# Kernel optimization log

Measured on AMD Instinct MI355X. Metric: run time of the kernel, lower is better.

The kernel has to match this reference:

```python
import jax, jax.numpy as jnp
import numpy as np

B, F, H, L, K = 16384, 1024, 1024, 256, 7

def _lin(key, fi, fo, lead=()):
    k1, k2 = jax.random.split(key)
    s = 1.0 / np.sqrt(fi)
    W = jax.random.uniform(k1, lead + (fi, fo), jnp.float32, -s, s)
    b = jax.random.uniform(k2, lead + (fo,), jnp.float32, -s, s)
    return W, b

def setup_inputs() -> dict:
    ks = jax.random.split(jax.random.key(0), 16)
    x = jax.random.normal(ks[0], (B, F), jnp.float32)
    t = jax.random.randint(ks[1], (B,), 0, K, jnp.int32)
    y = jax.random.normal(ks[2], (B,), jnp.float32)
    d = jax.random.normal(ks[3], (B,), jnp.float32)
    tw0, tb0 = _lin(ks[4], F, L)
    tw1, tb1 = _lin(ks[5], L, L)
    tw2, tb2 = _lin(ks[6], L, K)
    yw0, yb0 = _lin(ks[7], F, H)
    yw1, yb1 = _lin(ks[8], H, H)
    yhW, yhb = _lin(ks[9], H, 2, (K,))
    dw0, db0 = _lin(ks[10], F, H)
    dw1, db1 = _lin(ks[11], H, H)
    dhW, dhb = _lin(ks[12], H, 2, (K,))
    zw0, zb0 = _lin(ks[13], F + 2, H)
    zw1, zb1 = _lin(ks[14], H, H)
    zhW, zhb = _lin(ks[15], H, 2 * L, (K,))
    return dict(x=x, t=t, y=y, d=d, tw0=tw0, tb0=tb0, tw1=tw1, tb1=tb1, tw2=tw2, tb2=tb2,
                yw0=yw0, yb0=yb0, yw1=yw1, yb1=yb1, yhW=yhW, yhb=yhb,
                dw0=dw0, db0=db0, dw1=dw1, db1=db1, dhW=dhW, dhb=dhb,
                zw0=zw0, zb0=zb0, zw1=zw1, zb1=zb1, zhW=zhW, zhb=zhb)

def _mlp2(x, w0, b0, w1, b1):
    # FullyConnected([in, H, H], final_activation=ELU)
    return jax.nn.elu(jax.nn.elu(x @ w0 + b0) @ w1 + b1)

def _select(hidden, t, hW, hb):
    # dense compute of all K treatment heads, then per-row gather by t
    all_out = jnp.einsum('bh,khd->bkd', hidden, hW) + hb  # [B, K, D]
    return jnp.take_along_axis(all_out, t[:, None, None], axis=1)[:, 0]

def _normal_head(sel):
    # pyro NormalNet head on a scalar outcome
    loc = jnp.clip(sel[:, 0:1], -1e6, 1e6)
    scale = jnp.minimum(jax.nn.softplus(sel[:, 1:2]) + 1e-3, 1e6)
    return loc, scale

def _diagnormal_head(sel):
    loc = jnp.clip(sel[:, :L], -100.0, 100.0)
    scale = jnp.minimum(jax.nn.softplus(sel[:, L:]) + 0.001, 100.0)
    return loc, scale

def reference(x, t, y, d, tw0, tb0, tw1, tb1, tw2, tb2,
              yw0, yb0, yw1, yb1, yhW, yhb,
              dw0, db0, dw1, db1, dhW, dhb,
              zw0, zb0, zw1, zb1, zhW, zhb):
    # t_nn: MultinormNet, ELU final activation then clamp(-10, 10)
    t_logits = jnp.clip(jax.nn.elu(_mlp2(x, tw0, tb0, tw1, tb1) @ tw2 + tb2), -10.0, 10.0)
    # y_dist(t, x)
    hy = _mlp2(x, yw0, yb0, yw1, yb1)
    y_loc, y_scale = _normal_head(_select(hy, t, yhW, yhb))
    # d_dist(t, x)
    hd = _mlp2(x, dw0, db0, dw1, db1)
    d_loc, d_scale = _normal_head(_select(hd, t, dhW, dhb))
    # z_dist(y, d, t, x): hidden from cat([y, d, x])
    hz = _mlp2(jnp.concatenate([y[:, None], d[:, None], x], axis=-1), zw0, zb0, zw1, zb1)
    z_loc, z_scale = _diagnormal_head(_select(hz, t, zhW, zhb))
    # [B, K + 4 + 2L]
    return jnp.concatenate([t_logits, y_loc, y_scale, d_loc, d_scale, z_loc, z_scale], axis=-1)
```

## Files before the change

kernel.cpp:

```cpp
#include <hip/hip_runtime.h>
#include <hip/hip_bf16.h>
#include <cstdint>
#include <cstddef>

typedef __hip_bfloat16 bf16;
typedef __bf16 bf16x8 __attribute__((ext_vector_type(8)));
typedef float f32x4 __attribute__((ext_vector_type(4)));

#define DEVFN static __device__ __forceinline__
#define SBAR() __builtin_amdgcn_s_barrier()
#define VMCNT(n) asm volatile("s_waitcnt vmcnt(" #n ")" ::: "memory")

DEVFN void async16(const void* g, void* l) {
  __builtin_amdgcn_global_load_lds(
      (const __attribute__((address_space(1))) uint32_t*)g,
      (__attribute__((address_space(3))) uint32_t*)l, 16, 0, 0);
}

DEVFN float eluf(float v) { return v > 0.f ? v : expm1f(v); }
DEVFN float softplusf(float x) {
  return x > 0.f ? x + log1pf(expf(-x)) : log1pf(expf(x));
}


DEVFN void stage_half(const bf16* p, int ld, bf16* reg, int tid) {
  async16(p, reg + tid * 8);
  async16(p + (size_t)64 * ld, reg + 4096 + tid * 8);
}

template <int PART>
DEVFN void stage_ht(const bf16* pA, const bf16* pB, int lda, int ldb,
                    bf16* lds, int tid, int t) {
  bf16* base = lds + (t & 1) * 32768;
  if constexpr (PART == 0)
    stage_half(pA + (size_t)t * 64, lda, base, tid);
  else if constexpr (PART == 1)
    stage_half(pA + (size_t)t * 64 + (size_t)128 * lda, lda, base + 8192, tid);
  else if constexpr (PART == 2)
    stage_half(pB + (size_t)t * 64, ldb, base + 16384, tid);
  else
    stage_half(pB + (size_t)t * 64 + (size_t)128 * ldb, ldb, base + 24576, tid);
}

template <int MB, int NB>
DEVFN void mfma4(f32x4 (&acc)[8][4], const bf16x8 (&af)[4][2],
                 const bf16x8 (&bv)[2][2]) {
#pragma unroll
  for (int mf = 0; mf < 4; ++mf)
#pragma unroll
    for (int nf = 0; nf < 2; ++nf) {
      acc[MB + mf][NB + nf] = __builtin_amdgcn_mfma_f32_16x16x32_bf16(
          af[mf][0], bv[nf][0], acc[MB + mf][NB + nf], 0, 0, 0);
      acc[MB + mf][NB + nf] = __builtin_amdgcn_mfma_f32_16x16x32_bf16(
          af[mf][1], bv[nf][1], acc[MB + mf][NB + nf], 0, 0, 0);
    }
}

DEVFN void quad_phases(const bf16* Ab, const bf16* Bb, int cs0, int cs1,
                       f32x4 (&acc)[8][4], const bf16* pA, const bf16* pB,
                       int lda, int ldb, bf16* lds, int tid,
                       int t, bool st1, bool st2, int vmend) {
  bf16x8 af[4][2], b0[2][2], b1[2][2];
#pragma unroll
  for (int mf = 0; mf < 4; ++mf) {
    af[mf][0] = *(const bf16x8*)(Ab + mf * 1024 + cs0);
    af[mf][1] = *(const bf16x8*)(Ab + mf * 1024 + cs1);
  }
#pragma unroll
  for (int nf = 0; nf < 2; ++nf) {
    b0[nf][0] = *(const bf16x8*)(Bb + nf * 1024 + cs0);
    b0[nf][1] = *(const bf16x8*)(Bb + nf * 1024 + cs1);
  }
  if (st1) stage_ht<3>(pA, pB, lda, ldb, lds, tid, t + 1);
  SBAR();
  __builtin_amdgcn_s_setprio(1);
  mfma4<0, 0>(acc, af, b0);
  __builtin_amdgcn_s_setprio(0);
  SBAR();
#pragma unroll
  for (int nf = 0; nf < 2; ++nf) {
    b1[nf][0] = *(const bf16x8*)(Bb + (2 + nf) * 1024 + cs0);
    b1[nf][1] = *(const bf16x8*)(Bb + (2 + nf) * 1024 + cs1);
  }
  if (st1) stage_ht<1>(pA, pB, lda, ldb, lds, tid, t + 1);
  SBAR();
  __builtin_amdgcn_s_setprio(1);
  mfma4<0, 2>(acc, af, b1);
  __builtin_amdgcn_s_setprio(0);
  SBAR();
#pragma unroll
  for (int mf = 0; mf < 4; ++mf) {
    af[mf][0] = *(const bf16x8*)(Ab + (4 + mf) * 1024 + cs0);
    af[mf][1] = *(const bf16x8*)(Ab + (4 + mf) * 1024 + cs1);
  }
  if (st2) stage_ht<2>(pA, pB, lda, ldb, lds, tid, t + 2);
  SBAR();
  __builtin_amdgcn_s_setprio(1);
  mfma4<4, 0>(acc, af, b0);
  __builtin_amdgcn_s_setprio(0);
  SBAR();
  if (st2) stage_ht<0>(pA, pB, lda, ldb, lds, tid, t + 2);
  SBAR();
  __builtin_amdgcn_s_setprio(1);
  mfma4<4, 2>(acc, af, b1);
  __builtin_amdgcn_s_setprio(0);
  if (vmend == 0) { VMCNT(0); }
  else if (vmend > 0) { VMCNT(4); }
  SBAR();
}

DEVFN void gemm256(const bf16* pA, const bf16* pB, int lda, int ldb, int NT,
                   bf16* lds, int tid, int wm, int wn, int quad, int l15,
                   f32x4 (&acc)[8][4]) {
  const int k7 = l15 & 7;
  const int cs0 = (quad ^ k7) * 8;
  const int cs1 = cs0 ^ 32;
  const bf16* Abase = lds + wm * 8192 + l15 * 64;
  const bf16* Bbase = lds + 16384 + (wn >> 1) * 8192 + ((wn & 1) * 64 + l15) * 64;
  stage_ht<0>(pA, pB, lda, ldb, lds, tid, 0);
  stage_ht<1>(pA, pB, lda, ldb, lds, tid, 0);
  stage_ht<2>(pA, pB, lda, ldb, lds, tid, 0);
  stage_ht<3>(pA, pB, lda, ldb, lds, tid, 0);
  stage_ht<2>(pA, pB, lda, ldb, lds, tid, 1);
  stage_ht<0>(pA, pB, lda, ldb, lds, tid, 1);
  VMCNT(4);
  SBAR();
  const int NI = NT >> 1;
  for (int j = 0; j < NI; ++j) {
    const bool last = (j == NI - 1);
    const int a = 2 * j;
    quad_phases(Abase, Bbase, cs0, cs1, acc, pA, pB, lda, ldb, lds, tid,
                a, true, !last, last ? 0 : 4);
    quad_phases(Abase + 32768, Bbase + 32768, cs0, cs1, acc, pA, pB, lda, ldb,
                lds, tid, a + 1, !last, !last, last ? -1 : 4);
  }
}

template <int NAH, int NBH, int NFB>
DEVFN void kloop32(const bf16* (&gA)[NAH], const bf16* (&gB)[NBH], bf16* As,
                   bf16* Bs, int tid, const bf16* aBase, const bf16* bBase,
                   int colsel, f32x4 (&acc)[4][NFB], int kiters) {
  for (int kt = 0; kt < kiters; ++kt) {
#pragma unroll
    for (int c = 0; c < NAH; ++c) async16(gA[c], As + c * 2048 + tid * 8);
#pragma unroll
    for (int c = 0; c < NBH; ++c) async16(gB[c], Bs + c * 2048 + tid * 8);
#pragma unroll
    for (int c = 0; c < NAH; ++c) gA[c] += 32;
#pragma unroll
    for (int c = 0; c < NBH; ++c) gB[c] += 32;
    __syncthreads();
    bf16x8 af[4], bfv[NFB];
#pragma unroll
    for (int r = 0; r < 4; ++r) af[r] = *(const bf16x8*)(aBase + r * 512 + colsel);
#pragma unroll
    for (int c = 0; c < NFB; ++c) bfv[c] = *(const bf16x8*)(bBase + c * 512 + colsel);
#pragma unroll
    for (int r = 0; r < 4; ++r)
#pragma unroll
      for (int c = 0; c < NFB; ++c)
        acc[r][c] = __builtin_amdgcn_mfma_f32_16x16x32_bf16(af[r], bfv[c], acc[r][c], 0, 0, 0);
    __syncthreads();
  }
}

DEVFN int swz_scol(int tid) { return (((tid & 3) ^ ((tid >> 3) & 3)) * 8); }
DEVFN int swz_colsel(int quad, int l15) { return ((quad ^ ((l15 >> 1) & 3)) * 8); }

DEVFN void transpose_tile(const float* src, bf16* dst, int R, int C, int bx, int by) {
  __shared__ float tile[32][33];
  const int c0 = bx * 32, r0 = by * 32;
  const int tx = threadIdx.x & 31, ty = threadIdx.x >> 5;
#pragma unroll
  for (int rr = ty; rr < 32; rr += 8)
    tile[rr][tx] = src[(size_t)(r0 + rr) * C + c0 + tx];
  __syncthreads();
#pragma unroll
  for (int rr = ty; rr < 32; rr += 8)
    dst[(size_t)(c0 + rr) * R + r0 + tx] = __float2bfloat16(tile[tx][rr]);
}

__global__ __launch_bounds__(256) void prep_all_k(
    const float* __restrict__ x, bf16* __restrict__ xb,
    const float* __restrict__ yw0, const float* __restrict__ dw0,
    const float* __restrict__ zw0, const float* __restrict__ tw0,
    bf16* __restrict__ BtL1,
    const float* __restrict__ yw1, const float* __restrict__ dw1,
    const float* __restrict__ zw1, bf16* __restrict__ BtL2,
    const float* __restrict__ tw1, bf16* __restrict__ tw1t,
    const float* __restrict__ zhW, bf16* __restrict__ zhWt,
    const float* __restrict__ yb0, const float* __restrict__ db0,
    const float* __restrict__ zb0, const float* __restrict__ tb0,
    const float* __restrict__ yb1, const float* __restrict__ db1,
    const float* __restrict__ zb1,
    float* __restrict__ biasAll, float* __restrict__ r0All,
    float* __restrict__ r1All, float* __restrict__ biasL2,
    const int* __restrict__ t, int* __restrict__ cnt, int* __restrict__ seg,
    int* __restrict__ rank, int* __restrict__ sids) {
  int l = blockIdx.x;
  if (l < 8192) {
    size_t i = ((size_t)l * 256 + threadIdx.x) * 8;
    float4 v0 = *(const float4*)(x + i);
    float4 v1 = *(const float4*)(x + i + 4);
    union { bf16 h[8]; uint4 u; } o;
    o.h[0] = __float2bfloat16(v0.x); o.h[1] = __float2bfloat16(v0.y);
    o.h[2] = __float2bfloat16(v0.z); o.h[3] = __float2bfloat16(v0.w);
    o.h[4] = __float2bfloat16(v1.x); o.h[5] = __float2bfloat16(v1.y);
    o.h[6] = __float2bfloat16(v1.z); o.h[7] = __float2bfloat16(v1.w);
    *(uint4*)(xb + i) = o.u;
    return;
  }
  l -= 8192;
  if (l < 4096) {
    int z = l >> 10, rem = l & 1023, bx = rem & 31, by = rem >> 5;
    const float* src = (z == 0) ? yw0 : (z == 1) ? dw0 : (z == 2) ? zw0 + 2048 : tw0;
    int C = (z == 3) ? 256 : 1024;
    if (bx * 32 < C)
      transpose_tile(src, BtL1 + (size_t)z * 1024 * 1024, 1024, C, bx, by);
    return;
  }
  l -= 4096;
  if (l < 3072) {
    int z = l >> 10, rem = l & 1023, bx = rem & 31, by = rem >> 5;
    const float* src = (z == 0) ? yw1 : (z == 1) ? dw1 : zw1;
    transpose_tile(src, BtL2 + (size_t)z * 1024 * 1024, 1024, 1024, bx, by);
    return;
  }
  l -= 3072;
  if (l < 64) {
    transpose_tile(tw1, tw1t, 256, 256, l & 7, l >> 3);
    return;
  }
  l -= 64;
  if (l < 3584) {
    int z = l >> 9, rem = l & 511, bx = rem & 15, by = rem >> 4;
    transpose_tile(zhW + (size_t)z * 1024 * 512, zhWt + (size_t)z * 512 * 1024,
                   1024, 512, bx, by);
    return;
  }
  l -= 3584;
  if (l < 13) {
    int i = l * 256 + threadIdx.x;
    if (i >= 3328) return;
    float b;
    if (i < 1024) b = yb0[i];
    else if (i < 2048) b = db0[i - 1024];
    else if (i < 3072) b = zb0[i - 2048];
    else b = tb0[i - 3072];
    biasAll[i] = b;
    bool inz = (i >= 2048 && i < 3072);
    r0All[i] = inz ? zw0[i - 2048] : 0.f;
    r1All[i] = inz ? zw0[1024 + (i - 2048)] : 0.f;
    if (i < 3072)
      biasL2[i] = (i < 1024) ? yb1[i] : (i < 2048) ? db1[i - 1024] : zb1[i - 2048];
    return;
  }
  {
    __shared__ int h[8], sseg[8];
    const int tid = threadIdx.x;
    if (tid < 8) h[tid] = 0;
    __syncthreads();
    const int base = tid * 64;
    int lc[7] = {0, 0, 0, 0, 0, 0, 0};
    for (int i = 0; i < 64; ++i) lc[t[base + i]]++;
    int myoff[7];
#pragma unroll
    for (int k = 0; k < 7; ++k) myoff[k] = atomicAdd(&h[k], lc[k]);
    __syncthreads();
    if (tid == 0) {
      int s = 0;
      for (int k = 0; k < 7; ++k) { sseg[k] = s; s += h[k]; }
      sseg[7] = s;
    }
    __syncthreads();
    if (tid < 7) { cnt[tid] = h[tid]; seg[tid] = sseg[tid]; }
    if (tid == 7) seg[7] = sseg[7];
    int cur[7];
#pragma unroll
    for (int k = 0; k < 7; ++k) cur[k] = sseg[k] + myoff[k];
    for (int i = 0; i < 64; ++i) {
      int b = base + i, k = t[b];
      int r = cur[k]++;
      rank[b] = r;
      sids[r] = b;
    }
  }
}

__global__ __launch_bounds__(512, 1) void gemm_l1_k(
    const bf16* __restrict__ A, const bf16* __restrict__ Bt,
    const float* __restrict__ biasAll, const float* __restrict__ r0All,
    const float* __restrict__ r1All, const float* __restrict__ yv,
    const float* __restrict__ dv, bf16* __restrict__ a1y,
    bf16* __restrict__ a1d, bf16* __restrict__ a1z, bf16* __restrict__ ht1) {
  __shared__ bf16 lds[65536];
  const int tid = threadIdx.x, lane = tid & 63, wid = tid >> 6;
  const int wm = wid >> 2, wn = wid & 3, quad = lane >> 4, l15 = lane & 15;
  const int id = blockIdx.x;
  const int xcd = id & 7, lid = id >> 3;
  const int mt = xcd * 8 + (lid & 7), nt = lid >> 3;
  const int bm0 = mt * 256, bn0 = nt * 256;
  const int srow = tid >> 3, scol = ((tid & 7) ^ ((tid >> 3) & 7)) * 8;
  const bf16* pA = A + (size_t)(bm0 + srow) * 1024 + scol;
  const bf16* pB = Bt + (size_t)(bn0 + srow) * 1024 + scol;
  f32x4 acc[8][4] = {};
  gemm256(pA, pB, 1024, 1024, 16, lds, tid, wm, wn, quad, l15, acc);

  const int g = nt >> 2;
  bf16* dst = (g == 0) ? a1y : (g == 1) ? a1d : (g == 2) ? a1z : ht1;
  const int ldc = (g == 3) ? 256 : 1024;
  const int colb = bn0 - g * 1024;
  float bv[4], z0[4], z1[4];
#pragma unroll
  for (int nf = 0; nf < 4; ++nf) {
    int gn = bn0 + wn * 64 + nf * 16 + l15;
    bv[nf] = biasAll[gn]; z0[nf] = r0All[gn]; z1[nf] = r1All[gn];
  }
#pragma unroll
  for (int mf = 0; mf < 8; ++mf) {
    const int rbase = bm0 + wm * 128 + mf * 16 + quad * 4;
    const float4 y4 = *(const float4*)(yv + rbase);
    const float4 d4 = *(const float4*)(dv + rbase);
#pragma unroll
    for (int q = 0; q < 4; ++q) {
      const float yy = (&y4.x)[q], dd = (&d4.x)[q];
      const size_t ro = (size_t)(rbase + q) * ldc + colb + wn * 64;
#pragma unroll
      for (int nf = 0; nf < 4; ++nf) {
        float v = acc[mf][nf][q] + bv[nf] + yy * z0[nf] + dd * z1[nf];
        dst[ro + nf * 16 + l15] = __float2bfloat16(eluf(v));
      }
    }
  }
}

__global__ __launch_bounds__(512, 1) void gemm_l2t_k(
    const bf16* __restrict__ a1y, const bf16* __restrict__ a1d,
    const bf16* __restrict__ a1z, const bf16* __restrict__ ht1,
    const bf16* __restrict__ BtL2, const bf16* __restrict__ tw1t,
    const float* __restrict__ biasL2, const float* __restrict__ tb1,
    bf16* __restrict__ hyd, bf16* __restrict__ hzg, bf16* __restrict__ ht2,
    const int* __restrict__ rank) {
  __shared__ bf16 lds[65536];
  const int tid = threadIdx.x, lane = tid & 63, wid = tid >> 6;
  const int wm = wid >> 2, wn = wid & 3, quad = lane >> 4, l15 = lane & 15;
  const int id = blockIdx.x;
  int bm0, bn0, Ka, g;
  const bf16 *Aptr, *Bptr;
  if (id < 768) {
    const int xcd = id & 7, lid = id >> 3;
    const int mt = xcd * 8 + (lid & 7), nt = lid >> 3;
    bm0 = mt * 256; bn0 = nt * 256; Ka = 1024;
    g = nt >> 2;
    Aptr = (g == 0) ? a1y : (g == 1) ? a1d : a1z;
    Bptr = BtL2;
  } else {
    const int local = id - 768;
    bm0 = local * 256; bn0 = 0; Ka = 256;
    g = 3; Aptr = ht1; Bptr = tw1t;
  }
  const int srow = tid >> 3, scol = ((tid & 7) ^ ((tid >> 3) & 7)) * 8;
  const bf16* pA = Aptr + (size_t)(bm0 + srow) * Ka + scol;
  const bf16* pB = Bptr + (size_t)(bn0 + srow) * Ka + scol;
  f32x4 acc[8][4] = {};
  gemm256(pA, pB, Ka, Ka, Ka >> 6, lds, tid, wm, wn, quad, l15, acc);

  const float* bias = (g == 3) ? tb1 : biasL2;
  float bv[4];
#pragma unroll
  for (int nf = 0; nf < 4; ++nf) bv[nf] = bias[bn0 + wn * 64 + nf * 16 + l15];
#pragma unroll
  for (int mf = 0; mf < 8; ++mf) {
#pragma unroll
    for (int q = 0; q < 4; ++q) {
      const int gm = bm0 + wm * 128 + mf * 16 + quad * 4 + q;
      bf16* dst; size_t rowoff;
      if (g == 2) { dst = hzg; rowoff = (size_t)rank[gm] * 1024 + (size_t)(bn0 - 2048); }
      else if (g == 3) { dst = ht2; rowoff = (size_t)gm * 256; }
      else { dst = hyd; rowoff = (size_t)gm * 2048 + bn0; }
#pragma unroll
      for (int nf = 0; nf < 4; ++nf) {
        float v = acc[mf][nf][q] + bv[nf];
        dst[rowoff + wn * 64 + nf * 16 + l15] = __float2bfloat16(eluf(v));
      }
    }
  }
}

#define ZMT 28
#define ZB (7 * ZMT * 8)
__global__ __launch_bounds__(256) void tail_k(
    const bf16* __restrict__ hzg, const bf16* __restrict__ zhWt,
    const float* __restrict__ zhb, const int* __restrict__ seg,
    const int* __restrict__ cnts, const int* __restrict__ sids,
    const bf16* __restrict__ hyd, const bf16* __restrict__ ht2,
    const int* __restrict__ t, const float* __restrict__ yhW,
    const float* __restrict__ yhb, const float* __restrict__ dhW,
    const float* __restrict__ dhb, const float* __restrict__ tw2,
    const float* __restrict__ tb2, float* __restrict__ out) {
  __shared__ bf16 As[128 * 32];
  __shared__ bf16 Bs[64 * 32];
  const int tid = threadIdx.x, lane = tid & 63, wid = tid >> 6;
  const int wv = wid, quad = lane >> 4, l15 = lane & 15;
  if (blockIdx.x < ZB) {
    const int kb = blockIdx.x / (ZMT * 8);
    const int r = blockIdx.x % (ZMT * 8);
    const int cnt = cnts[kb];
    const int bm0 = (r >> 3) * 128;
    if (bm0 >= cnt) return;
    const int n0 = (r & 7) * 64;
    const int wm = wid >> 1, wn = wid & 1;
    const int base = seg[kb];
    const int sr = tid >> 2, scol = swz_scol(tid);
    const bf16* gA[2];
    const bf16* gB[1];
#pragma unroll
    for (int c = 0; c < 2; ++c) {
      int rr = bm0 + c * 64 + sr;
      if (rr >= cnt) rr = cnt - 1;
      gA[c] = hzg + (size_t)(base + rr) * 1024 + scol;
    }
    gB[0] = zhWt + (size_t)kb * 512 * 1024 + (size_t)(n0 + sr) * 1024 + scol;
    const bf16* aBase = &As[(wm * 64 + l15) * 32];
    const bf16* bBase = &Bs[(wn * 32 + l15) * 32];
    const int colsel = swz_colsel(quad, l15);
    f32x4 acc[4][2] = {};
    kloop32<2, 1, 2>(gA, gB, As, Bs, tid, aBase, bBase, colsel, acc, 32);
    const float* bias = zhb + (size_t)kb * 512;
    float bv[2]; int gnn[2];
#pragma unroll
    for (int c = 0; c < 2; ++c) {
      gnn[c] = n0 + wn * 32 + c * 16 + l15;
      bv[c] = bias[gnn[c]];
    }
#pragma unroll
    for (int r2 = 0; r2 < 4; ++r2)
#pragma unroll
      for (int q = 0; q < 4; ++q) {
        int lm = bm0 + wm * 64 + r2 * 16 + quad * 4 + q;
        if (lm < cnt) {
          int gm = sids[base + lm];
          size_t ob = (size_t)gm * 523 + 11;
#pragma unroll
          for (int c = 0; c < 2; ++c) {
            float v = acc[r2][c][q] + bv[c];
            int n = gnn[c];
            out[ob + n] = (n < 256) ? fminf(fmaxf(v, -100.f), 100.f)
                                    : fminf(softplusf(v) + 0.001f, 100.f);
          }
        }
      }
    return;
  }
  const int hid = blockIdx.x - ZB;
  if (hid < 4096) {
    const int b = hid * 4 + wv;
    const int tb = t[b];
    const float* yW = yhW + (size_t)tb * 2048;
    const float* dW = dhW + (size_t)tb * 2048;
    float s0 = 0.f, s1 = 0.f, s2 = 0.f, s3 = 0.f;
    for (int i = lane; i < 1024; i += 64) {
      float a = __bfloat162float(hyd[(size_t)b * 2048 + i]);
      float c = __bfloat162float(hyd[(size_t)b * 2048 + 1024 + i]);
      s0 += a * yW[2 * i]; s1 += a * yW[2 * i + 1];
      s2 += c * dW[2 * i]; s3 += c * dW[2 * i + 1];
    }
#pragma unroll
    for (int off = 32; off > 0; off >>= 1) {
      s0 += __shfl_down(s0, off); s1 += __shfl_down(s1, off);
      s2 += __shfl_down(s2, off); s3 += __shfl_down(s3, off);
    }
    if (lane == 0) {
      size_t o = (size_t)b * 523;
      out[o + 7] = fminf(fmaxf(s0 + yhb[tb * 2], -1e6f), 1e6f);
      out[o + 8] = fminf(softplusf(s1 + yhb[tb * 2 + 1]) + 1e-3f, 1e6f);
      out[o + 9] = fminf(fmaxf(s2 + dhb[tb * 2], -1e6f), 1e6f);
      out[o + 10] = fminf(softplusf(s3 + dhb[tb * 2 + 1]) + 1e-3f, 1e6f);
    }
  } else {
    const int b = (hid - 4096) * 4 + wv;
    float h[4];
#pragma unroll
    for (int j = 0; j < 4; ++j)
      h[j] = __bfloat162float(ht2[(size_t)b * 256 + lane * 4 + j]);
    float pp[7];
#pragma unroll
    for (int kk = 0; kk < 7; ++kk) {
      float s = 0.f;
#pragma unroll
      for (int j = 0; j < 4; ++j) s += h[j] * tw2[(lane * 4 + j) * 7 + kk];
      pp[kk] = s;
    }
#pragma unroll
    for (int kk = 0; kk < 7; ++kk)
#pragma unroll
      for (int off = 32; off > 0; off >>= 1) pp[kk] += __shfl_down(pp[kk], off);
    if (lane == 0) {
#pragma unroll
      for (int kk = 0; kk < 7; ++kk) {
        float v = eluf(pp[kk] + tb2[kk]);
        out[(size_t)b * 523 + kk] = fminf(fmaxf(v, -10.f), 10.f);
      }
    }
  }
}

extern "C" void kernel_launch(void* const* d_in, const int* in_sizes, int n_in,
                              void* d_out, int out_size, void* d_ws, size_t ws_size,
                              hipStream_t stream) {
  const float* x   = (const float*)d_in[0];
  const int*   t   = (const int*)d_in[1];
  const float* yv  = (const float*)d_in[2];
  const float* dv  = (const float*)d_in[3];
  const float* tw0 = (const float*)d_in[4];
  const float* tb0 = (const float*)d_in[5];
  const float* tw1 = (const float*)d_in[6];
  const float* tb1 = (const float*)d_in[7];
  const float* tw2 = (const float*)d_in[8];
  const float* tb2 = (const float*)d_in[9];
  const float* yw0 = (const float*)d_in[10];
  const float* yb0 = (const float*)d_in[11];
  const float* yw1 = (const float*)d_in[12];
  const float* yb1 = (const float*)d_in[13];
  const float* yhW = (const float*)d_in[14];
  const float* yhb = (const float*)d_in[15];
  const float* dw0 = (const float*)d_in[16];
  const float* db0 = (const float*)d_in[17];
  const float* dw1 = (const float*)d_in[18];
  const float* db1 = (const float*)d_in[19];
  const float* dhW = (const float*)d_in[20];
  const float* dhb = (const float*)d_in[21];
  const float* zw0 = (const float*)d_in[22];
  const float* zb0 = (const float*)d_in[23];
  const float* zw1 = (const float*)d_in[24];
  const float* zb1 = (const float*)d_in[25];
  const float* zhW = (const float*)d_in[26];
  const float* zhb = (const float*)d_in[27];
  float* out = (float*)d_out;

  const int B = 16384;
  char* p = (char*)d_ws;
  auto take = [&](size_t bytes) {
    char* r = p;
    p += (bytes + 255) & ~(size_t)255;
    return r;
  };
  bf16*  BtL1    = (bf16*)take((size_t)3328 * 1024 * 2);
  bf16*  BtL2    = (bf16*)take((size_t)3072 * 1024 * 2);
  bf16*  tw1t    = (bf16*)take((size_t)256 * 256 * 2);
  bf16*  zhWt    = (bf16*)take((size_t)7 * 512 * 1024 * 2);
  float* biasAll = (float*)take(3328 * 4);
  float* r0All   = (float*)take(3328 * 4);
  float* r1All   = (float*)take(3328 * 4);
  float* biasL2  = (float*)take(3072 * 4);
  int*   cnt     = (int*)take(8 * 4);
  int*   seg     = (int*)take(8 * 4);
  int*   rank    = (int*)take((size_t)B * 4);
  int*   sids    = (int*)take((size_t)B * 4);
  bf16*  xb      = (bf16*)take((size_t)B * 1024 * 2);
  bf16*  a1y     = (bf16*)take((size_t)B * 1024 * 2);
  bf16*  a1d     = (bf16*)take((size_t)B * 1024 * 2);
  bf16*  a1z     = (bf16*)take((size_t)B * 1024 * 2);
  bf16*  ht1     = (bf16*)take((size_t)B * 256 * 2);
  bf16*  hyd     = (bf16*)take((size_t)B * 2048 * 2);
  bf16*  ht2     = (bf16*)take((size_t)B * 256 * 2);
  bf16*  hzg     = xb;

  prep_all_k<<<19022, 256, 0, stream>>>(x, xb, yw0, dw0, zw0, tw0, BtL1,
                                        yw1, dw1, zw1, BtL2, tw1, tw1t, zhW, zhWt,
                                        yb0, db0, zb0, tb0, yb1, db1, zb1,
                                        biasAll, r0All, r1All, biasL2,
                                        t, cnt, seg, rank, sids);
  gemm_l1_k<<<832, 512, 0, stream>>>(xb, BtL1, biasAll, r0All, r1All,
                                     yv, dv, a1y, a1d, a1z, ht1);
  gemm_l2t_k<<<832, 512, 0, stream>>>(a1y, a1d, a1z, ht1, BtL2, tw1t,
                                      biasL2, tb1, hyd, hzg, ht2, rank);
  tail_k<<<ZB + 8192, 256, 0, stream>>>(hzg, zhWt, zhb, seg, cnt, sids,
                                        hyd, ht2, t, yhW, yhb, dhW, dhb,
                                        tw2, tb2, out);
}
```

Measured before the change: 673.5 us.

## Run z-head grouped GEMM through the pipelined 256x256 tile path in a separate kernel

The per-treatment z-head GEMM, which used a simple 128x64 tile loop with syncthreads, now reuses the double-buffered 256x256 gemm256 pipeline in its own 512-thread kernel. To allow that, the staging helpers take four precomputed row pointers instead of base plus stride, so the ragged row count can be clamped per row. The y/d/t heads are split into a second launch. The larger tiles raise data reuse and MFMA density, but they add padding waste on ragged groups, leave fewer blocks, and cost an extra kernel launch.

```diff
diff --git a/kernel.cpp b/kernel.cpp
--- a/kernel.cpp
+++ b/kernel.cpp
@@ -23,23 +23,24 @@
 }
 
 
-DEVFN void stage_half(const bf16* p, int ld, bf16* reg, int tid) {
-  async16(p, reg + tid * 8);
-  async16(p + (size_t)64 * ld, reg + 4096 + tid * 8);
+DEVFN void stage_half2(const bf16* p0, const bf16* p64, bf16* dst, int tid) {
+  async16(p0, dst + tid * 8);
+  async16(p64, dst + 4096 + tid * 8);
 }
 
 template <int PART>
-DEVFN void stage_ht(const bf16* pA, const bf16* pB, int lda, int ldb,
+DEVFN void stage_ht(const bf16* const (&pAr)[4], const bf16* const (&pBr)[4],
                     bf16* lds, int tid, int t) {
   bf16* base = lds + (t & 1) * 32768;
+  const size_t o = (size_t)t * 64;
   if constexpr (PART == 0)
-    stage_half(pA + (size_t)t * 64, lda, base, tid);
+    stage_half2(pAr[0] + o, pAr[1] + o, base, tid);
   else if constexpr (PART == 1)
-    stage_half(pA + (size_t)t * 64 + (size_t)128 * lda, lda, base + 8192, tid);
+    stage_half2(pAr[2] + o, pAr[3] + o, base + 8192, tid);
   else if constexpr (PART == 2)
-    stage_half(pB + (size_t)t * 64, ldb, base + 16384, tid);
+    stage_half2(pBr[0] + o, pBr[1] + o, base + 16384, tid);
   else
-    stage_half(pB + (size_t)t * 64 + (size_t)128 * ldb, ldb, base + 24576, tid);
+    stage_half2(pBr[2] + o, pBr[3] + o, base + 24576, tid);
 }
 
 template <int MB, int NB>
@@ -57,8 +58,8 @@
 }
 
 DEVFN void quad_phases(const bf16* Ab, const bf16* Bb, int cs0, int cs1,
-                       f32x4 (&acc)[8][4], const bf16* pA, const bf16* pB,
-                       int lda, int ldb, bf16* lds, int tid,
+                       f32x4 (&acc)[8][4], const bf16* const (&pAr)[4],
+                       const bf16* const (&pBr)[4], bf16* lds, int tid,
                        int t, bool st1, bool st2, int vmend) {
   bf16x8 af[4][2], b0[2][2], b1[2][2];
 #pragma unroll
@@ -71,7 +72,7 @@
     b0[nf][0] = *(const bf16x8*)(Bb + nf * 1024 + cs0);
     b0[nf][1] = *(const bf16x8*)(Bb + nf * 1024 + cs1);
   }
-  if (st1) stage_ht<3>(pA, pB, lda, ldb, lds, tid, t + 1);
+  if (st1) stage_ht<3>(pAr, pBr, lds, tid, t + 1);
   SBAR();
   __builtin_amdgcn_s_setprio(1);
   mfma4<0, 0>(acc, af, b0);
@@ -82,7 +83,7 @@
     b1[nf][0] = *(const bf16x8*)(Bb + (2 + nf) * 1024 + cs0);
     b1[nf][1] = *(const bf16x8*)(Bb + (2 + nf) * 1024 + cs1);
   }
-  if (st1) stage_ht<1>(pA, pB, lda, ldb, lds, tid, t + 1);
+  if (st1) stage_ht<1>(pAr, pBr, lds, tid, t + 1);
   SBAR();
   __builtin_amdgcn_s_setprio(1);
   mfma4<0, 2>(acc, af, b1);
@@ -93,13 +94,13 @@
     af[mf][0] = *(const bf16x8*)(Ab + (4 + mf) * 1024 + cs0);
     af[mf][1] = *(const bf16x8*)(Ab + (4 + mf) * 1024 + cs1);
   }
-  if (st2) stage_ht<2>(pA, pB, lda, ldb, lds, tid, t + 2);
+  if (st2) stage_ht<2>(pAr, pBr, lds, tid, t + 2);
   SBAR();
   __builtin_amdgcn_s_setprio(1);
   mfma4<4, 0>(acc, af, b0);
   __builtin_amdgcn_s_setprio(0);
   SBAR();
-  if (st2) stage_ht<0>(pA, pB, lda, ldb, lds, tid, t + 2);
+  if (st2) stage_ht<0>(pAr, pBr, lds, tid, t + 2);
   SBAR();
   __builtin_amdgcn_s_setprio(1);
   mfma4<4, 2>(acc, af, b1);
@@ -109,63 +110,32 @@
   SBAR();
 }
 
-DEVFN void gemm256(const bf16* pA, const bf16* pB, int lda, int ldb, int NT,
-                   bf16* lds, int tid, int wm, int wn, int quad, int l15,
-                   f32x4 (&acc)[8][4]) {
+DEVFN void gemm256(const bf16* const (&pAr)[4], const bf16* const (&pBr)[4],
+                   int NT, bf16* lds, int tid, int wm, int wn, int quad,
+                   int l15, f32x4 (&acc)[8][4]) {
   const int k7 = l15 & 7;
   const int cs0 = (quad ^ k7) * 8;
   const int cs1 = cs0 ^ 32;
   const bf16* Abase = lds + wm * 8192 + l15 * 64;
   const bf16* Bbase = lds + 16384 + (wn >> 1) * 8192 + ((wn & 1) * 64 + l15) * 64;
-  stage_ht<0>(pA, pB, lda, ldb, lds, tid, 0);
-  stage_ht<1>(pA, pB, lda, ldb, lds, tid, 0);
-  stage_ht<2>(pA, pB, lda, ldb, lds, tid, 0);
-  stage_ht<3>(pA, pB, lda, ldb, lds, tid, 0);
-  stage_ht<2>(pA, pB, lda, ldb, lds, tid, 1);
-  stage_ht<0>(pA, pB, lda, ldb, lds, tid, 1);
+  stage_ht<0>(pAr, pBr, lds, tid, 0);
+  stage_ht<1>(pAr, pBr, lds, tid, 0);
+  stage_ht<2>(pAr, pBr, lds, tid, 0);
+  stage_ht<3>(pAr, pBr, lds, tid, 0);
+  stage_ht<2>(pAr, pBr, lds, tid, 1);
+  stage_ht<0>(pAr, pBr, lds, tid, 1);
   VMCNT(4);
   SBAR();
   const int NI = NT >> 1;
   for (int j = 0; j < NI; ++j) {
     const bool last = (j == NI - 1);
     const int a = 2 * j;
-    quad_phases(Abase, Bbase, cs0, cs1, acc, pA, pB, lda, ldb, lds, tid,
+    quad_phases(Abase, Bbase, cs0, cs1, acc, pAr, pBr, lds, tid,
                 a, true, !last, last ? 0 : 4);
-    quad_phases(Abase + 32768, Bbase + 32768, cs0, cs1, acc, pA, pB, lda, ldb,
-                lds, tid, a + 1, !last, !last, last ? -1 : 4);
-  }
-}
-
-template <int NAH, int NBH, int NFB>
-DEVFN void kloop32(const bf16* (&gA)[NAH], const bf16* (&gB)[NBH], bf16* As,
-                   bf16* Bs, int tid, const bf16* aBase, const bf16* bBase,
-                   int colsel, f32x4 (&acc)[4][NFB], int kiters) {
-  for (int kt = 0; kt < kiters; ++kt) {
-#pragma unroll
-    for (int c = 0; c < NAH; ++c) async16(gA[c], As + c * 2048 + tid * 8);
-#pragma unroll
-    for (int c = 0; c < NBH; ++c) async16(gB[c], Bs + c * 2048 + tid * 8);
-#pragma unroll
-    for (int c = 0; c < NAH; ++c) gA[c] += 32;
-#pragma unroll
-    for (int c = 0; c < NBH; ++c) gB[c] += 32;
-    __syncthreads();
-    bf16x8 af[4], bfv[NFB];
-#pragma unroll
-    for (int r = 0; r < 4; ++r) af[r] = *(const bf16x8*)(aBase + r * 512 + colsel);
-#pragma unroll
-    for (int c = 0; c < NFB; ++c) bfv[c] = *(const bf16x8*)(bBase + c * 512 + colsel);
-#pragma unroll
-    for (int r = 0; r < 4; ++r)
-#pragma unroll
-      for (int c = 0; c < NFB; ++c)
-        acc[r][c] = __builtin_amdgcn_mfma_f32_16x16x32_bf16(af[r], bfv[c], acc[r][c], 0, 0, 0);
-    __syncthreads();
-  }
-}
-
-DEVFN int swz_scol(int tid) { return (((tid & 3) ^ ((tid >> 3) & 3)) * 8); }
-DEVFN int swz_colsel(int quad, int l15) { return ((quad ^ ((l15 >> 1) & 3)) * 8); }
+    quad_phases(Abase + 32768, Bbase + 32768, cs0, cs1, acc, pAr, pBr, lds,
+                tid, a + 1, !last, !last, last ? -1 : 4);
+  }
+}
 
 DEVFN void transpose_tile(const float* src, bf16* dst, int R, int C, int bx, int by) {
   __shared__ float tile[32][33];
@@ -301,10 +271,15 @@
   const int mt = xcd * 8 + (lid & 7), nt = lid >> 3;
   const int bm0 = mt * 256, bn0 = nt * 256;
   const int srow = tid >> 3, scol = ((tid & 7) ^ ((tid >> 3) & 7)) * 8;
-  const bf16* pA = A + (size_t)(bm0 + srow) * 1024 + scol;
-  const bf16* pB = Bt + (size_t)(bn0 + srow) * 1024 + scol;
+  const bf16* pAr[4];
+  const bf16* pBr[4];
+#pragma unroll
+  for (int k = 0; k < 4; ++k) {
+    pAr[k] = A + (size_t)(bm0 + srow + k * 64) * 1024 + scol;
+    pBr[k] = Bt + (size_t)(bn0 + srow + k * 64) * 1024 + scol;
+  }
   f32x4 acc[8][4] = {};
-  gemm256(pA, pB, 1024, 1024, 16, lds, tid, wm, wn, quad, l15, acc);
+  gemm256(pAr, pBr, 16, lds, tid, wm, wn, quad, l15, acc);
 
   const int g = nt >> 2;
   bf16* dst = (g == 0) ? a1y : (g == 1) ? a1d : (g == 2) ? a1z : ht1;
@@ -360,10 +335,15 @@
     g = 3; Aptr = ht1; Bptr = tw1t;
   }
   const int srow = tid >> 3, scol = ((tid & 7) ^ ((tid >> 3) & 7)) * 8;
-  const bf16* pA = Aptr + (size_t)(bm0 + srow) * Ka + scol;
-  const bf16* pB = Bptr + (size_t)(bn0 + srow) * Ka + scol;
+  const bf16* pAr[4];
+  const bf16* pBr[4];
+#pragma unroll
+  for (int k = 0; k < 4; ++k) {
+    pAr[k] = Aptr + (size_t)(bm0 + srow + k * 64) * Ka + scol;
+    pBr[k] = Bptr + (size_t)(bn0 + srow + k * 64) * Ka + scol;
+  }
   f32x4 acc[8][4] = {};
-  gemm256(pA, pB, Ka, Ka, Ka >> 6, lds, tid, wm, wn, quad, l15, acc);
+  gemm256(pAr, pBr, Ka >> 6, lds, tid, wm, wn, quad, l15, acc);
 
   const float* bias = (g == 3) ? tb1 : biasL2;
   float bv[4];
@@ -387,72 +367,70 @@
   }
 }
 
-#define ZMT 28
-#define ZB (7 * ZMT * 8)
-__global__ __launch_bounds__(256) void tail_k(
+#define ZMT2 14
+__global__ __launch_bounds__(512, 1) void tail_z_k(
     const bf16* __restrict__ hzg, const bf16* __restrict__ zhWt,
     const float* __restrict__ zhb, const int* __restrict__ seg,
     const int* __restrict__ cnts, const int* __restrict__ sids,
+    float* __restrict__ out) {
+  __shared__ bf16 lds[65536];
+  const int tid = threadIdx.x, lane = tid & 63, wid = tid >> 6;
+  const int wm = wid >> 2, wn = wid & 3, quad = lane >> 4, l15 = lane & 15;
+  const int id = blockIdx.x;
+  const int kb = id / (ZMT2 * 2), rem = id % (ZMT2 * 2);
+  const int cnt = cnts[kb];
+  const int bm0 = (rem >> 1) * 256;
+  if (bm0 >= cnt) return;
+  const int bn0 = (rem & 1) * 256;
+  const int base = seg[kb];
+  const int srow = tid >> 3, scol = ((tid & 7) ^ ((tid >> 3) & 7)) * 8;
+  const bf16* pAr[4];
+  const bf16* pBr[4];
+#pragma unroll
+  for (int k = 0; k < 4; ++k) {
+    int r = bm0 + srow + k * 64;
+    if (r >= cnt) r = cnt - 1;
+    pAr[k] = hzg + (size_t)(base + r) * 1024 + scol;
+    pBr[k] = zhWt + (size_t)kb * 512 * 1024 +
+             (size_t)(bn0 + srow + k * 64) * 1024 + scol;
+  }
+  f32x4 acc[8][4] = {};
+  gemm256(pAr, pBr, 16, lds, tid, wm, wn, quad, l15, acc);
+
+  const float* bias = zhb + (size_t)kb * 512;
+  float bv[4]; int gnn[4];
+#pragma unroll
+  for (int nf = 0; nf < 4; ++nf) {
+    gnn[nf] = bn0 + wn * 64 + nf * 16 + l15;
+    bv[nf] = bias[gnn[nf]];
+  }
+#pragma unroll
+  for (int mf = 0; mf < 8; ++mf) {
+#pragma unroll
+    for (int q = 0; q < 4; ++q) {
+      const int lm = bm0 + wm * 128 + mf * 16 + quad * 4 + q;
+      if (lm < cnt) {
+        const size_t ob = (size_t)sids[base + lm] * 523 + 11;
+#pragma unroll
+        for (int nf = 0; nf < 4; ++nf) {
+          float v = acc[mf][nf][q] + bv[nf];
+          out[ob + gnn[nf]] = (gnn[nf] < 256)
+                                  ? fminf(fmaxf(v, -100.f), 100.f)
+                                  : fminf(softplusf(v) + 0.001f, 100.f);
+        }
+      }
+    }
+  }
+}
+
+__global__ __launch_bounds__(256) void tail_heads_k(
     const bf16* __restrict__ hyd, const bf16* __restrict__ ht2,
     const int* __restrict__ t, const float* __restrict__ yhW,
     const float* __restrict__ yhb, const float* __restrict__ dhW,
     const float* __restrict__ dhb, const float* __restrict__ tw2,
     const float* __restrict__ tb2, float* __restrict__ out) {
-  __shared__ bf16 As[128 * 32];
-  __shared__ bf16 Bs[64 * 32];
-  const int tid = threadIdx.x, lane = tid & 63, wid = tid >> 6;
-  const int wv = wid, quad = lane >> 4, l15 = lane & 15;
-  if (blockIdx.x < ZB) {
-    const int kb = blockIdx.x / (ZMT * 8);
-    const int r = blockIdx.x % (ZMT * 8);
-    const int cnt = cnts[kb];
-    const int bm0 = (r >> 3) * 128;
-    if (bm0 >= cnt) return;
-    const int n0 = (r & 7) * 64;
-    const int wm = wid >> 1, wn = wid & 1;
-    const int base = seg[kb];
-    const int sr = tid >> 2, scol = swz_scol(tid);
-    const bf16* gA[2];
-    const bf16* gB[1];
-#pragma unroll
-    for (int c = 0; c < 2; ++c) {
-      int rr = bm0 + c * 64 + sr;
-      if (rr >= cnt) rr = cnt - 1;
-      gA[c] = hzg + (size_t)(base + rr) * 1024 + scol;
-    }
-    gB[0] = zhWt + (size_t)kb * 512 * 1024 + (size_t)(n0 + sr) * 1024 + scol;
-    const bf16* aBase = &As[(wm * 64 + l15) * 32];
-    const bf16* bBase = &Bs[(wn * 32 + l15) * 32];
-    const int colsel = swz_colsel(quad, l15);
-    f32x4 acc[4][2] = {};
-    kloop32<2, 1, 2>(gA, gB, As, Bs, tid, aBase, bBase, colsel, acc, 32);
-    const float* bias = zhb + (size_t)kb * 512;
-    float bv[2]; int gnn[2];
-#pragma unroll
-    for (int c = 0; c < 2; ++c) {
-      gnn[c] = n0 + wn * 32 + c * 16 + l15;
-      bv[c] = bias[gnn[c]];
-    }
-#pragma unroll
-    for (int r2 = 0; r2 < 4; ++r2)
-#pragma unroll
-      for (int q = 0; q < 4; ++q) {
-        int lm = bm0 + wm * 64 + r2 * 16 + quad * 4 + q;
-        if (lm < cnt) {
-          int gm = sids[base + lm];
-          size_t ob = (size_t)gm * 523 + 11;
-#pragma unroll
-          for (int c = 0; c < 2; ++c) {
-            float v = acc[r2][c][q] + bv[c];
-            int n = gnn[c];
-            out[ob + n] = (n < 256) ? fminf(fmaxf(v, -100.f), 100.f)
-                                    : fminf(softplusf(v) + 0.001f, 100.f);
-          }
-        }
-      }
-    return;
-  }
-  const int hid = blockIdx.x - ZB;
+  const int lane = threadIdx.x & 63, wv = threadIdx.x >> 6;
+  const int hid = blockIdx.x;
   if (hid < 4096) {
     const int b = hid * 4 + wv;
     const int tb = t[b];
@@ -575,7 +553,7 @@
                                      yv, dv, a1y, a1d, a1z, ht1);
   gemm_l2t_k<<<832, 512, 0, stream>>>(a1y, a1d, a1z, ht1, BtL2, tw1t,
                                       biasL2, tb1, hyd, hzg, ht2, rank);
-  tail_k<<<ZB + 8192, 256, 0, stream>>>(hzg, zhWt, zhb, seg, cnt, sids,
-                                        hyd, ht2, t, yhW, yhb, dhW, dhb,
-                                        tw2, tb2, out);
-}
+  tail_z_k<<<7 * ZMT2 * 2, 512, 0, stream>>>(hzg, zhWt, zhb, seg, cnt, sids, out);
+  tail_heads_k<<<8192, 256, 0, stream>>>(hyd, ht2, t, yhW, yhb, dhW, dhb,
+                                         tw2, tb2, out);
+}
```

Result: slower. 784.0 us (+16.4%).
